# Kernel tuning notes

Hardware: AMD Instinct MI355X
Metric: run time of the kernel (lower is better)

## Reference

```python
import jax, jax.numpy as jnp
import numpy as np

ATT = 64   # attention_size (becomes number of split chunks / effective heads)
NH = 16    # num_heads (becomes chunk width / effective head dim)


def setup_inputs() -> dict:
    key = jax.random.key(0)
    ks = jax.random.split(key, 9)
    B, T, E = 4, 1024, 1024
    AH = ATT * NH  # 1024
    s = 0.02
    return {
        "x": jax.random.normal(ks[0], (B, T, E), jnp.float32),
        "Wq": jax.random.normal(ks[1], (E, AH), jnp.float32) * s,
        "bq": jax.random.normal(ks[2], (AH,), jnp.float32) * s,
        "Wk": jax.random.normal(ks[3], (E, AH), jnp.float32) * s,
        "bk": jax.random.normal(ks[4], (AH,), jnp.float32) * s,
        "Wv": jax.random.normal(ks[5], (E, AH), jnp.float32) * s,
        "bv": jax.random.normal(ks[6], (AH,), jnp.float32) * s,
        "Wo": jax.random.normal(ks[7], (AH, E), jnp.float32) * s,
        "bo": jax.random.normal(ks[8], (E,), jnp.float32) * s,
    }


def reference(x, Wq, bq, Wk, bk, Wv, bv, Wo, bo):
    B, T, E = x.shape
    A, H = ATT, NH

    q = x @ Wq + bq  # [B,T,A*H]
    k = x @ Wk + bk
    v = x @ Wv + bv

    # torch.split(m, num_heads, dim=2) -> A chunks of width H; cat along dim 0
    def split_cat(m):
        # [B,T,A,H] -> [A,B,T,H] -> [A*B,T,H]
        return m.reshape(B, T, A, H).transpose(2, 0, 1, 3).reshape(A * B, T, H)

    q = split_cat(q)
    k = split_cat(k)
    v = split_cat(v)

    scores = jnp.einsum('bqh,bkh->bqk', q, k) / (A ** 0.5)  # [A*B,T,T]
    attn = jax.nn.softmax(scores, axis=-1)
    z = jnp.einsum('bqk,bkh->bqh', attn, v)  # [A*B,T,H]

    # faithful to torch: contiguous [A*B,T,H] viewed as [B, T, A*H] (no un-permute)
    z = z.reshape(B, T, A * H)
    return z @ Wo + bo
```

## Files before the change

kernel.cpp:

```cpp
#include <hip/hip_runtime.h>
#include <hip/hip_bf16.h>


typedef __bf16 bf16_t;
typedef bf16_t bf16x8 __attribute__((ext_vector_type(8)));
typedef float f32x4 __attribute__((ext_vector_type(4)));

#define SCALE_LOG2E 0.18033688011112042f

__device__ __forceinline__ void async16(const bf16_t* g, void* l) {
    __builtin_amdgcn_global_load_lds(
        (const __attribute__((address_space(1))) unsigned int*)g,
        (__attribute__((address_space(3))) unsigned int*)l,
        16, 0, 0);
}

__global__ __launch_bounds__(256) void cast_f32_bf16(
    const float* __restrict__ in, bf16_t* __restrict__ out, int n8)
{
    int i = blockIdx.x * 256 + threadIdx.x;
    if (i >= n8) return;
    const float4* p = (const float4*)in + (size_t)i * 2;
    float4 a = p[0], b = p[1];
    bf16x8 o;
    o[0] = (bf16_t)a.x; o[1] = (bf16_t)a.y; o[2] = (bf16_t)a.z; o[3] = (bf16_t)a.w;
    o[4] = (bf16_t)b.x; o[5] = (bf16_t)b.y; o[6] = (bf16_t)b.z; o[7] = (bf16_t)b.w;
    *((bf16x8*)out + i) = o;
}

__global__ __launch_bounds__(256) void transpose_cast(
    const float* __restrict__ W0, const float* __restrict__ W1,
    const float* __restrict__ W2, const float* __restrict__ W3,
    bf16_t* __restrict__ out)
{
    __shared__ float st[32][33];
    const float* W = (blockIdx.z == 0) ? W0 : (blockIdx.z == 1) ? W1
                   : (blockIdx.z == 2) ? W2 : W3;
    bf16_t* o = out + (size_t)blockIdx.z * 1024 * 1024;
    const int n0 = blockIdx.x * 32, k0 = blockIdx.y * 32;
    const int t = threadIdx.x;
    const int r = t >> 3, c4 = (t & 7) * 4;
    float4 v = *(const float4*)(W + (size_t)(k0 + r) * 1024 + n0 + c4);
    st[r][c4 + 0] = v.x; st[r][c4 + 1] = v.y; st[r][c4 + 2] = v.z; st[r][c4 + 3] = v.w;
    __syncthreads();
    bf16_t tmp[4] __attribute__((aligned(8)));
    #pragma unroll
    for (int i = 0; i < 4; ++i) tmp[i] = (bf16_t)st[c4 + i][r];
    *(uint2*)(o + (size_t)(n0 + r) * 1024 + k0 + c4) = *(const uint2*)tmp;
}

template<bool FUSED>
__global__ __launch_bounds__(256, 3) void gemm_glds(
    const bf16_t* __restrict__ A, const bf16_t* __restrict__ Bt,
    const float* __restrict__ b0, const float* __restrict__ b1,
    const float* __restrict__ b2,
    bf16_t* __restrict__ Qo, bf16_t* __restrict__ Ko, bf16_t* __restrict__ Vo,
    float* __restrict__ Fo)
{
    const int K = 1024;
    __shared__ __align__(16) bf16_t As[128 * 32];
    __shared__ __align__(16) bf16_t Bs[128 * 32];

    const int tid  = threadIdx.x;
    const int wave = tid >> 6;
    const int lane = tid & 63;
    const int quad = lane >> 4;
    const int l16  = lane & 15;
    const int m0 = blockIdx.y * 128;
    const int n0 = blockIdx.x * 128;
    const int wm = (wave >> 1) * 64;
    const int wn = (wave & 1) * 64;

    int goffA[2], goffB[2];
    #pragma unroll
    for (int j = 0; j < 2; ++j) {
        const int row = j * 64 + (tid >> 2);
        const int cl  = (tid & 3) ^ ((row >> 1) & 3);
        goffA[j] = (m0 + row) * K + cl * 8;
        goffB[j] = (n0 + row) * K + cl * 8;
    }
    const int ldsoff = wave * 1024;

    f32x4 acc[4][4] = {};
    const int sw = (l16 >> 1) & 3;

    for (int k0 = 0; k0 < K; k0 += 32) {
        #pragma unroll
        for (int j = 0; j < 2; ++j) {
            async16(A + goffA[j] + k0, (char*)As + j * 4096 + ldsoff);
            async16(Bt + goffB[j] + k0, (char*)Bs + j * 4096 + ldsoff);
        }
        __syncthreads();

        bf16x8 af[4], bfr[4];
        #pragma unroll
        for (int mt = 0; mt < 4; ++mt)
            af[mt] = *(const bf16x8*)(&As[(wm + mt * 16 + l16) * 32 + (quad ^ sw) * 8]);
        #pragma unroll
        for (int nt = 0; nt < 4; ++nt)
            bfr[nt] = *(const bf16x8*)(&Bs[(wn + nt * 16 + l16) * 32 + (quad ^ sw) * 8]);
        #pragma unroll
        for (int mt = 0; mt < 4; ++mt)
            #pragma unroll
            for (int nt = 0; nt < 4; ++nt)
                acc[mt][nt] = __builtin_amdgcn_mfma_f32_16x16x32_bf16(
                    af[mt], bfr[nt], acc[mt][nt], 0, 0, 0);
        __syncthreads();
    }

    if (FUSED) {
        const int sel = n0 >> 10;
        const float* bias = (sel == 0) ? b0 : (sel == 1) ? b1 : b2;
        bf16_t* Cout      = (sel == 0) ? Qo : (sel == 1) ? Ko : Vo;
        const float scl   = (sel == 1) ? SCALE_LOG2E : 1.0f;
        const int nb = n0 & 1023;
        #pragma unroll
        for (int nt = 0; nt < 4; ++nt) {
            const int n = nb + wn + nt * 16 + l16;
            const float bb = bias[n];
            #pragma unroll
            for (int mt = 0; mt < 4; ++mt)
                #pragma unroll
                for (int i = 0; i < 4; ++i) {
                    const int m = m0 + wm + mt * 16 + quad * 4 + i;
                    Cout[(size_t)m * 1024 + n] = (bf16_t)((acc[mt][nt][i] + bb) * scl);
                }
        }
    } else {
        #pragma unroll
        for (int nt = 0; nt < 4; ++nt) {
            const int n = n0 + wn + nt * 16 + l16;
            const float bb = b0[n];
            #pragma unroll
            for (int mt = 0; mt < 4; ++mt)
                #pragma unroll
                for (int i = 0; i < 4; ++i) {
                    const int m = m0 + wm + mt * 16 + quad * 4 + i;
                    Fo[(size_t)m * 1024 + n] = acc[mt][nt][i] + bb;
                }
        }
    }
}

__global__ __launch_bounds__(256, 4) void attn_kernel(
    const bf16_t* __restrict__ Q, const bf16_t* __restrict__ K,
    const bf16_t* __restrict__ V, bf16_t* __restrict__ Z)
{
    __shared__ __align__(16) bf16_t Pw[4][64 * 72];
    __shared__ __align__(16) bf16_t Vt[16 * 72];

    const int tid  = threadIdx.x;
    const int wave = tid >> 6;
    const int lane = tid & 63;
    const int quad = lane >> 4;
    const int l16  = lane & 15;
    const int hd = blockIdx.x >> 2;
    const int qc = blockIdx.x & 3;
    const int a = hd >> 2, b = hd & 3;
    const int col0 = a * 16;
    const int qbase = qc * 256 + wave * 64;

    bf16x8 qf[4] = {};
    if (quad < 2) {
        #pragma unroll
        for (int mt = 0; mt < 4; ++mt)
            qf[mt] = *(const bf16x8*)(Q +
                (size_t)(b * 1024 + qbase + mt * 16 + l16) * 1024 + col0 + quad * 8);
    }

    bf16x8 ones;
    #pragma unroll
    for (int j = 0; j < 8; ++j) ones[j] = (bf16_t)1.0f;

    f32x4 zacc[4] = {};
    f32x4 lacc[4] = {};
    bf16_t* myP = &Pw[wave][0];

    for (int j0 = 0; j0 < 1024; j0 += 64) {
        __syncthreads();
        {
            const int r  = tid >> 2;
            const int dq = (tid & 3) * 4;
            uint2 vv = *(const uint2*)(V +
                (size_t)(b * 1024 + j0 + r) * 1024 + col0 + dq);
            bf16_t t4[4] __attribute__((aligned(8)));
            *(uint2*)t4 = vv;
            const int kcol = (r & 15) * 4 + (r >> 4);
            #pragma unroll
            for (int ii = 0; ii < 4; ++ii)
                Vt[(dq + ii) * 72 + kcol] = t4[ii];
        }
        bf16x8 kf[4] = {};
        if (quad < 2) {
            #pragma unroll
            for (int nt = 0; nt < 4; ++nt)
                kf[nt] = *(const bf16x8*)(K +
                    (size_t)(b * 1024 + j0 + nt * 16 + l16) * 1024 + col0 + quad * 8);
        }
        __syncthreads();

        #pragma unroll
        for (int mt = 0; mt < 4; ++mt) {
            f32x4 s[4];
            #pragma unroll
            for (int nt = 0; nt < 4; ++nt) {
                f32x4 zc = {0.f, 0.f, 0.f, 0.f};
                s[nt] = __builtin_amdgcn_mfma_f32_16x16x32_bf16(qf[mt], kf[nt], zc, 0, 0, 0);
            }
            #pragma unroll
            for (int i = 0; i < 4; ++i) {
                bf16_t pk4[4] __attribute__((aligned(8)));
                #pragma unroll
                for (int nt = 0; nt < 4; ++nt)
                    pk4[nt] = (bf16_t)exp2f(s[nt][i]);
                *(uint2*)(myP + (mt * 16 + quad * 4 + i) * 72 + l16 * 4) = *(const uint2*)pk4;
            }
        }

        #pragma unroll
        for (int kt = 0; kt < 2; ++kt) {
            bf16x8 vf = *(const bf16x8*)(&Vt[l16 * 72 + kt * 32 + quad * 8]);
            #pragma unroll
            for (int mt = 0; mt < 4; ++mt) {
                bf16x8 pf = *(const bf16x8*)(myP + (mt * 16 + l16) * 72 + kt * 32 + quad * 8);
                zacc[mt] = __builtin_amdgcn_mfma_f32_16x16x32_bf16(pf, vf, zacc[mt], 0, 0, 0);
                lacc[mt] = __builtin_amdgcn_mfma_f32_16x16x32_bf16(pf, ones, lacc[mt], 0, 0, 0);
            }
        }
    }

    #pragma unroll
    for (int mt = 0; mt < 4; ++mt) {
        #pragma unroll
        for (int i = 0; i < 4; ++i) {
            const float inv = 1.0f / lacc[mt][i];
            const int t = qbase + mt * 16 + quad * 4 + i;
            Z[((size_t)hd * 1024 + t) * 16 + l16] = (bf16_t)(zacc[mt][i] * inv);
        }
    }
}

extern "C" void kernel_launch(void* const* d_in, const int* in_sizes, int n_in,
                              void* d_out, int out_size, void* d_ws, size_t ws_size,
                              hipStream_t stream) {
    const float* x  = (const float*)d_in[0];
    const float* Wq = (const float*)d_in[1];
    const float* bq = (const float*)d_in[2];
    const float* Wk = (const float*)d_in[3];
    const float* bk = (const float*)d_in[4];
    const float* Wv = (const float*)d_in[5];
    const float* bv = (const float*)d_in[6];
    const float* Wo = (const float*)d_in[7];
    const float* bo = (const float*)d_in[8];
    float* out = (float*)d_out;

    char* ws = (char*)d_ws;
    bf16_t* x_bf = (bf16_t*)(ws);
    bf16_t* Wt   = (bf16_t*)(ws + (8u << 20));
    bf16_t* Qb   = (bf16_t*)(ws + (16u << 20));
    bf16_t* Kb   = (bf16_t*)(ws + (24u << 20));
    bf16_t* Vb   = (bf16_t*)(ws + (32u << 20));
    bf16_t* Zb   = (bf16_t*)(ws + (40u << 20));
    bf16_t* WtO  = Wt + (size_t)3 * 1024 * 1024;

    cast_f32_bf16<<<dim3(2048), dim3(256), 0, stream>>>(x, x_bf, 524288);
    transpose_cast<<<dim3(32, 32, 4), dim3(256), 0, stream>>>(Wq, Wk, Wv, Wo, Wt);

    gemm_glds<true><<<dim3(24, 32), dim3(256), 0, stream>>>(
        x_bf, Wt, bq, bk, bv, Qb, Kb, Vb, nullptr);

    attn_kernel<<<dim3(1024), dim3(256), 0, stream>>>(Qb, Kb, Vb, Zb);

    gemm_glds<false><<<dim3(8, 32), dim3(256), 0, stream>>>(
        Zb, WtO, bo, nullptr, nullptr, nullptr, nullptr, nullptr, out);
}
```

Measured before the change: 221.7 us.

## Prefetch next K/V tiles in attention, cheaper bf16 pack, smaller out-proj tiles

The attention loop now loads the next iteration's V row and K fragments into registers during the current compute, so global latency overlaps the MFMA and exp work. The bf16 conversion of the exp2 results is done with a manual round-half-up and byte perm instead of per-element casts. The output projection GEMM is templated to use 64-row M tiles, doubling its grid to 512 blocks for better CU occupancy on 256 CUs. This adds register pressure from the prefetch buffers, and the manual rounding does not round ties to even.

```diff
diff --git a/kernel.cpp b/kernel.cpp
--- a/kernel.cpp
+++ b/kernel.cpp
@@ -49,7 +49,7 @@
     *(uint2*)(o + (size_t)(n0 + r) * 1024 + k0 + c4) = *(const uint2*)tmp;
 }
 
-template<bool FUSED>
+template<bool FUSED, int MT>
 __global__ __launch_bounds__(256, 3) void gemm_glds(
     const bf16_t* __restrict__ A, const bf16_t* __restrict__ Bt,
     const float* __restrict__ b0, const float* __restrict__ b1,
@@ -58,51 +58,60 @@
     float* __restrict__ Fo)
 {
     const int K = 1024;
-    __shared__ __align__(16) bf16_t As[128 * 32];
+    __shared__ __align__(16) bf16_t As[MT * 32];
     __shared__ __align__(16) bf16_t Bs[128 * 32];
+
+    constexpr int NTPW = (MT == 128) ? 4 : 2;
+    constexpr int JA   = MT / 64;
 
     const int tid  = threadIdx.x;
     const int wave = tid >> 6;
     const int lane = tid & 63;
     const int quad = lane >> 4;
     const int l16  = lane & 15;
-    const int m0 = blockIdx.y * 128;
+    const int m0 = blockIdx.y * MT;
     const int n0 = blockIdx.x * 128;
-    const int wm = (wave >> 1) * 64;
-    const int wn = (wave & 1) * 64;
-
-    int goffA[2], goffB[2];
+    const int wm = (MT == 128) ? (wave >> 1) * 64 : 0;
+    const int wn = (MT == 128) ? (wave & 1) * 64 : wave * 32;
+
+    int goffA[JA], goffB[2];
+    #pragma unroll
+    for (int j = 0; j < JA; ++j) {
+        const int row = j * 64 + (tid >> 2);
+        const int cl  = (tid & 3) ^ ((row >> 1) & 3);
+        goffA[j] = (m0 + row) * K + cl * 8;
+    }
     #pragma unroll
     for (int j = 0; j < 2; ++j) {
         const int row = j * 64 + (tid >> 2);
         const int cl  = (tid & 3) ^ ((row >> 1) & 3);
-        goffA[j] = (m0 + row) * K + cl * 8;
         goffB[j] = (n0 + row) * K + cl * 8;
     }
     const int ldsoff = wave * 1024;
 
-    f32x4 acc[4][4] = {};
+    f32x4 acc[4][NTPW] = {};
     const int sw = (l16 >> 1) & 3;
 
     for (int k0 = 0; k0 < K; k0 += 32) {
         #pragma unroll
-        for (int j = 0; j < 2; ++j) {
+        for (int j = 0; j < JA; ++j)
             async16(A + goffA[j] + k0, (char*)As + j * 4096 + ldsoff);
+        #pragma unroll
+        for (int j = 0; j < 2; ++j)
             async16(Bt + goffB[j] + k0, (char*)Bs + j * 4096 + ldsoff);
-        }
-        __syncthreads();
-
-        bf16x8 af[4], bfr[4];
+        __syncthreads();
+
+        bf16x8 af[4], bfr[NTPW];
         #pragma unroll
         for (int mt = 0; mt < 4; ++mt)
             af[mt] = *(const bf16x8*)(&As[(wm + mt * 16 + l16) * 32 + (quad ^ sw) * 8]);
         #pragma unroll
-        for (int nt = 0; nt < 4; ++nt)
+        for (int nt = 0; nt < NTPW; ++nt)
             bfr[nt] = *(const bf16x8*)(&Bs[(wn + nt * 16 + l16) * 32 + (quad ^ sw) * 8]);
         #pragma unroll
         for (int mt = 0; mt < 4; ++mt)
             #pragma unroll
-            for (int nt = 0; nt < 4; ++nt)
+            for (int nt = 0; nt < NTPW; ++nt)
                 acc[mt][nt] = __builtin_amdgcn_mfma_f32_16x16x32_bf16(
                     af[mt], bfr[nt], acc[mt][nt], 0, 0, 0);
         __syncthreads();
@@ -115,7 +124,7 @@
         const float scl   = (sel == 1) ? SCALE_LOG2E : 1.0f;
         const int nb = n0 & 1023;
         #pragma unroll
-        for (int nt = 0; nt < 4; ++nt) {
+        for (int nt = 0; nt < NTPW; ++nt) {
             const int n = nb + wn + nt * 16 + l16;
             const float bb = bias[n];
             #pragma unroll
@@ -128,7 +137,7 @@
         }
     } else {
         #pragma unroll
-        for (int nt = 0; nt < 4; ++nt) {
+        for (int nt = 0; nt < NTPW; ++nt) {
             const int n = n0 + wn + nt * 16 + l16;
             const float bb = b0[n];
             #pragma unroll
@@ -172,31 +181,36 @@
     #pragma unroll
     for (int j = 0; j < 8; ++j) ones[j] = (bf16_t)1.0f;
 
+    const int r    = tid >> 2;
+    const int dq   = (tid & 3) * 4;
+    const int kcol = (r & 15) * 4 + (r >> 4);
+    const bf16_t* Vp = V + (size_t)(b * 1024 + r) * 1024 + col0 + dq;
+    const bf16_t* Kp = K + (size_t)(b * 1024 + l16) * 1024 + col0 + quad * 8;
+
+    uint2 vv = *(const uint2*)Vp;
+    bf16x8 kfp[4] = {};
+    if (quad < 2) {
+        #pragma unroll
+        for (int nt = 0; nt < 4; ++nt)
+            kfp[nt] = *(const bf16x8*)(Kp + (size_t)(nt * 16) * 1024);
+    }
+
     f32x4 zacc[4] = {};
     f32x4 lacc[4] = {};
     bf16_t* myP = &Pw[wave][0];
 
     for (int j0 = 0; j0 < 1024; j0 += 64) {
+        const int jn = j0 + 64;
         __syncthreads();
         {
-            const int r  = tid >> 2;
-            const int dq = (tid & 3) * 4;
-            uint2 vv = *(const uint2*)(V +
-                (size_t)(b * 1024 + j0 + r) * 1024 + col0 + dq);
             bf16_t t4[4] __attribute__((aligned(8)));
             *(uint2*)t4 = vv;
-            const int kcol = (r & 15) * 4 + (r >> 4);
             #pragma unroll
             for (int ii = 0; ii < 4; ++ii)
                 Vt[(dq + ii) * 72 + kcol] = t4[ii];
         }
-        bf16x8 kf[4] = {};
-        if (quad < 2) {
-            #pragma unroll
-            for (int nt = 0; nt < 4; ++nt)
-                kf[nt] = *(const bf16x8*)(K +
-                    (size_t)(b * 1024 + j0 + nt * 16 + l16) * 1024 + col0 + quad * 8);
-        }
+        if (jn < 1024)
+            vv = *(const uint2*)(Vp + (size_t)jn * 1024);
         __syncthreads();
 
         #pragma unroll
@@ -205,16 +219,25 @@
             #pragma unroll
             for (int nt = 0; nt < 4; ++nt) {
                 f32x4 zc = {0.f, 0.f, 0.f, 0.f};
-                s[nt] = __builtin_amdgcn_mfma_f32_16x16x32_bf16(qf[mt], kf[nt], zc, 0, 0, 0);
+                s[nt] = __builtin_amdgcn_mfma_f32_16x16x32_bf16(qf[mt], kfp[nt], zc, 0, 0, 0);
             }
             #pragma unroll
             for (int i = 0; i < 4; ++i) {
-                bf16_t pk4[4] __attribute__((aligned(8)));
-                #pragma unroll
-                for (int nt = 0; nt < 4; ++nt)
-                    pk4[nt] = (bf16_t)exp2f(s[nt][i]);
-                *(uint2*)(myP + (mt * 16 + quad * 4 + i) * 72 + l16 * 4) = *(const uint2*)pk4;
+                unsigned int u0 = __builtin_bit_cast(unsigned int, exp2f(s[0][i])) + 0x8000u;
+                unsigned int u1 = __builtin_bit_cast(unsigned int, exp2f(s[1][i])) + 0x8000u;
+                unsigned int u2 = __builtin_bit_cast(unsigned int, exp2f(s[2][i])) + 0x8000u;
+                unsigned int u3 = __builtin_bit_cast(unsigned int, exp2f(s[3][i])) + 0x8000u;
+                uint2 w;
+                w.x = __builtin_amdgcn_perm(u1, u0, 0x07060302u);
+                w.y = __builtin_amdgcn_perm(u3, u2, 0x07060302u);
+                *(uint2*)(myP + (mt * 16 + quad * 4 + i) * 72 + l16 * 4) = w;
             }
+        }
+
+        if (jn < 1024 && quad < 2) {
+            #pragma unroll
+            for (int nt = 0; nt < 4; ++nt)
+                kfp[nt] = *(const bf16x8*)(Kp + (size_t)(jn + nt * 16) * 1024);
         }
 
         #pragma unroll
@@ -266,11 +289,11 @@
     cast_f32_bf16<<<dim3(2048), dim3(256), 0, stream>>>(x, x_bf, 524288);
     transpose_cast<<<dim3(32, 32, 4), dim3(256), 0, stream>>>(Wq, Wk, Wv, Wo, Wt);
 
-    gemm_glds<true><<<dim3(24, 32), dim3(256), 0, stream>>>(
+    gemm_glds<true, 128><<<dim3(24, 32), dim3(256), 0, stream>>>(
         x_bf, Wt, bq, bk, bv, Qb, Kb, Vb, nullptr);
 
     attn_kernel<<<dim3(1024), dim3(256), 0, stream>>>(Qb, Kb, Vb, Zb);
 
-    gemm_glds<false><<<dim3(8, 32), dim3(256), 0, stream>>>(
+    gemm_glds<false, 64><<<dim3(8, 64), dim3(256), 0, stream>>>(
         Zb, WtO, bo, nullptr, nullptr, nullptr, nullptr, nullptr, out);
 }
```

After: 221.9 us. Within noise of the previous version (+0.1%).
